# Performance work log

Measured on AMD Instinct MI355X. Metric: run time of the kernel, lower is better.

The kernel has to match this reference:

```python
import jax, jax.numpy as jnp
import numpy as np

BATCH_SIZE = 512
N_PARTS = 4
TEMP_FAC = 0.1
D = 4096
EPS = 1e-6


def _static_indices():
    # bs and factor per the n_parts==4, batch_size!=12 branch
    bs = 4 * BATCH_SIZE
    factor = 10 * N_PARTS
    pos = np.arange(bs)
    active = pos[pos % (3 * N_PARTS) < N_PARTS]            # positions that contribute
    # i1..i6 = (pos + k*n_parts) % bs for k = 0..5
    I = (active[:, None] + np.arange(6)[None, :] * N_PARTS) % bs   # (P, 6)
    # denominator indices removed: (pos + k*n_parts) % bs for k = 0..factor*n_parts-1
    offs = (active[:, None] + np.arange(factor * N_PARTS)[None, :] * N_PARTS) % bs
    M = np.ones((active.shape[0], bs), dtype=np.float32)
    M[np.arange(active.shape[0])[:, None], offs] = 0.0     # (P, bs) denominator mask
    return I, M

_I, _M = _static_indices()
# symmetrical-loss pairs: (i1,i2),(i2,i3),(i1,i4),(i4,i5),(i5,i6),(i2,i5),(i3,i6)
_PAIRS = [(0, 1), (1, 2), (0, 3), (3, 4), (4, 5), (1, 4), (2, 5)]


def setup_inputs() -> dict:
    key = jax.random.key(0)
    reg_pred = jax.random.normal(key, (4 * BATCH_SIZE, D), dtype=jnp.float32)
    return {"reg_pred": reg_pred}


def reference(reg_pred):
    I = jnp.asarray(_I)
    M = jnp.asarray(_M)
    norms = jnp.linalg.norm(reg_pred, axis=1)              # (bs,)
    # torch CosineSimilarity: dot / max(||a||*||b||, eps)
    gram = reg_pred @ reg_pred.T                           # (bs, bs)
    S = gram / jnp.maximum(norms[:, None] * norms[None, :], EPS) / TEMP_FAC
    E = jnp.exp(S)                                         # (bs, bs)
    # denominator exp-sums for each anchor role k at each active position p
    Dsum = jnp.einsum('pkb,pb->pk', E[I], M)               # (P, 6)
    total = jnp.float32(0.0)
    for a, b in _PAIRS:
        num = S[I[:, a], I[:, b]]                          # (P,)
        en = jnp.exp(num)
        total = total + jnp.sum(-jnp.log(en / (en + Dsum[:, a]))
                                - jnp.log(en / (en + Dsum[:, b])))
    return total / (6 * BATCH_SIZE)
```

## Files before the change

kernel.cpp:

```cpp
#include <hip/hip_runtime.h>
#include <hip/hip_bf16.h>
#include <stdint.h>

#define NROWS 2048
#define DIM   4096
#define NACT  684
#define INV_TEMP 10.0f
#define NPANEL 32
#define NTILE64 528
#define NK 64
#define FP8_SCALE 16.0f
#define OUT_SCALE (INV_TEMP / 256.0f)

#define WAITCNT_VM0   0x0F70
#define WAITCNT_VM4   0x0F74
#define WAITCNT_VM8   0x0F78

typedef __attribute__((ext_vector_type(4))) float floatx4;
typedef __attribute__((ext_vector_type(16))) float floatx16;
typedef __attribute__((ext_vector_type(4))) int intx4;
typedef __attribute__((ext_vector_type(8))) int intx8;
typedef __attribute__((ext_vector_type(8))) short shortx8;
typedef __attribute__((ext_vector_type(8))) unsigned short ushortx8;

static __device__ __forceinline__ unsigned short f32_to_bf16(float f) {
  union { float f; unsigned int u; } v; v.f = f;
  unsigned int u = v.u;
  unsigned int r = u + 0x7fffu + ((u >> 16) & 1u);
  return (unsigned short)(r >> 16);
}
static __device__ __forceinline__ float bf16_to_f32(unsigned short u) {
  union { unsigned int u; float f; } v; v.u = ((unsigned int)u) << 16;
  return v.f;
}
static __device__ __forceinline__ unsigned short f32_to_f16(float f) {
  _Float16 h = (_Float16)f;
  union { _Float16 h; unsigned short u; } v; v.h = h;
  return v.u;
}
static __device__ __forceinline__ float f16_to_f32(unsigned short u) {
  union { unsigned short u; _Float16 h; } v; v.u = u;
  return (float)v.h;
}

static __device__ __forceinline__ void num_store(float* __restrict__ NUM, int R, int delta,
                                                 float v) {
  if (delta == 4) {
    const int qs[4]  = {0, 1, 3, 4};
    const int pas[4] = {0, 1, 3, 4};
#pragma unroll
    for (int u = 0; u < 4; u++) {
      const int aa = (R - 4 * pas[u]) & (NROWS - 1);
      if (aa % 12 < 4) NUM[((aa / 12) * 4 + (aa % 12)) * 7 + qs[u]] = v;
    }
  } else {
    const int qs[3]  = {2, 5, 6};
    const int pas[3] = {0, 1, 2};
#pragma unroll
    for (int u = 0; u < 3; u++) {
      const int aa = (R - 4 * pas[u]) & (NROWS - 1);
      if (aa % 12 < 4) NUM[((aa / 12) * 4 + (aa % 12)) * 7 + qs[u]] = v;
    }
  }
}

__global__ __launch_bounds__(256) void k_normconv_fp8(const float* __restrict__ X,
                                                      unsigned char* __restrict__ Yq,
                                                      float* __restrict__ T,
                                                      float* __restrict__ WS,
                                                      float* __restrict__ out) {
  const int row = blockIdx.x;
  if (threadIdx.x == 0) T[row] = 0.f;
  if (row == 0 && threadIdx.x == 64) *out = 0.f;
  if (row < NACT && threadIdx.x >= 192 && threadIdx.x < 198)
    WS[row * 6 + (threadIdx.x - 192)] = 0.f;
  const float4* xr = (const float4*)(X + (size_t)row * DIM);
  float4 v[4];
  float s = 0.f;
#pragma unroll
  for (int t = 0; t < 4; t++) {
    float4 w = xr[threadIdx.x + t * 256];
    v[t] = w;
    s += w.x * w.x + w.y * w.y + w.z * w.z + w.w * w.w;
  }
#pragma unroll
  for (int off = 32; off > 0; off >>= 1) s += __shfl_down(s, off, 64);
  __shared__ float wsum[4];
  if ((threadIdx.x & 63) == 0) wsum[threadIdx.x >> 6] = s;
  __syncthreads();
  const float total = wsum[0] + wsum[1] + wsum[2] + wsum[3];
  const float sc = FP8_SCALE / fmaxf(sqrtf(total), 1e-30f);
  unsigned int* yr = (unsigned int*)(Yq + (size_t)row * DIM);
#pragma unroll
  for (int t = 0; t < 4; t++) {
    float4 w = v[t];
    unsigned int r0 = __builtin_amdgcn_cvt_pk_fp8_f32(w.x * sc, w.y * sc, 0, false);
    r0 = __builtin_amdgcn_cvt_pk_fp8_f32(w.z * sc, w.w * sc, r0, true);
    yr[threadIdx.x + t * 256] = r0;
  }
}

__global__ __launch_bounds__(256) void k_gemm_full(const unsigned char* __restrict__ Yq,
                                                   float* __restrict__ T,
                                                   float* __restrict__ WS,
                                                   float* __restrict__ NUM) {
  __shared__ __attribute__((aligned(16))) unsigned char lds[6 * 8192];
  const int bid0 = blockIdx.x;
  const int t = (bid0 & 7) * 66 + (bid0 >> 3);
  int ti = 0, rem = t;
  while (rem >= NPANEL - ti) { rem -= NPANEL - ti; ti++; }
  const int tj = ti + rem;
  const int gr = ti * 64;
  const int gc = tj * 64;

  const int tid  = threadIdx.x;
  const int lane = tid & 63;
  const int wave = tid >> 6;
  const int wr = wave >> 1;
  const int wc = wave & 1;

  floatx16 acc = {0.f, 0.f, 0.f, 0.f, 0.f, 0.f, 0.f, 0.f,
                  0.f, 0.f, 0.f, 0.f, 0.f, 0.f, 0.f, 0.f};

  const int r2  = tid >> 2;
  const int c16 = tid & 3;
  const unsigned int swst = (unsigned)(((r2 >> 1) & 3) << 4);
  const unsigned int colst = ((unsigned)(c16 << 4)) ^ swst;
  const unsigned char* gA = Yq + (size_t)(gr + r2) * DIM + colst;
  const unsigned char* gB = Yq + (size_t)(gc + r2) * DIM + colst;

#define ISSUE(st, koff)                                                                  \
  do {                                                                                   \
    __builtin_amdgcn_global_load_lds(                                                    \
        (const __attribute__((address_space(1))) void*)(gA + (koff)),                    \
        (__attribute__((address_space(3))) void*)(lds + (st) * 8192 + tid * 16),         \
        16, 0, 0);                                                                       \
    __builtin_amdgcn_global_load_lds(                                                    \
        (const __attribute__((address_space(1))) void*)(gB + (koff)),                    \
        (__attribute__((address_space(3))) void*)(lds + (st) * 8192 + 4096 + tid * 16),  \
        16, 0, 0);                                                                       \
  } while (0)

#define COMPUTE(st)                                                                      \
  do {                                                                                   \
    const unsigned char* bA = lds + (st) * 8192;                                         \
    const unsigned char* bB = bA + 4096;                                                 \
    const unsigned int c0 = (unsigned)((lane >> 5) << 5);                                \
    const int rA = wr * 32 + (lane & 31);                                                \
    const int rB = wc * 32 + (lane & 31);                                                \
    const unsigned int swA = (unsigned)(((rA >> 1) & 3) << 4);                           \
    const unsigned int swB = (unsigned)(((rB >> 1) & 3) << 4);                           \
    const unsigned char* baseA = bA + rA * 64;                                           \
    const unsigned char* baseB = bB + rB * 64;                                           \
    intx4 alo = *(const intx4*)(baseA + (c0 ^ swA));                                     \
    intx4 ahi = *(const intx4*)(baseA + ((c0 ^ swA) ^ 16u));                             \
    intx4 blo = *(const intx4*)(baseB + (c0 ^ swB));                                     \
    intx4 bhi = *(const intx4*)(baseB + ((c0 ^ swB) ^ 16u));                             \
    intx8 af, bf;                                                                        \
    af[0] = alo[0]; af[1] = alo[1]; af[2] = alo[2]; af[3] = alo[3];                      \
    af[4] = ahi[0]; af[5] = ahi[1]; af[6] = ahi[2]; af[7] = ahi[3];                      \
    bf[0] = blo[0]; bf[1] = blo[1]; bf[2] = blo[2]; bf[3] = blo[3];                      \
    bf[4] = bhi[0]; bf[5] = bhi[1]; bf[6] = bhi[2]; bf[7] = bhi[3];                      \
    acc = __builtin_amdgcn_mfma_scale_f32_32x32x64_f8f6f4(                               \
        af, bf, acc, 0, 0, 0, 0x7F7F7F7F, 0, 0x7F7F7F7F);                                \
  } while (0)

  ISSUE(0, 0);
  ISSUE(1, 64);
  ISSUE(2, 128);
  ISSUE(3, 192);
#pragma unroll
  for (int p = 0; p < 32; p++) {
    const int a = (2 * p) % 6;
    if (p < 30) {
      const int na = (2 * p + 4) % 6;
      ISSUE(na, (2 * p + 4) * 64);
      ISSUE(na + 1, (2 * p + 5) * 64);
      __builtin_amdgcn_s_waitcnt(WAITCNT_VM8);
    } else if (p == 30) {
      __builtin_amdgcn_s_waitcnt(WAITCNT_VM4);
    } else {
      __builtin_amdgcn_s_waitcnt(WAITCNT_VM0);
    }
    __builtin_amdgcn_sched_barrier(0);
    __builtin_amdgcn_s_barrier();
    __builtin_amdgcn_s_setprio(1);
    COMPUTE(a);
    COMPUTE(a + 1);
    __builtin_amdgcn_s_setprio(0);
    if (p < 31) {
      __builtin_amdgcn_s_barrier();
      __builtin_amdgcn_sched_barrier(0);
    }
  }

#undef ISSUE
#undef COMPUTE

  float* tileE   = (float*)lds;
  float* colpart = (float*)(lds + 16640);
  __syncthreads();

  {
    const int col = wc * 32 + (lane & 31);
    float evsum = 0.f;
#pragma unroll
    for (int i = 0; i < 16; i++) {
      const int row = wr * 32 + (i & 3) + 8 * (i >> 2) + 4 * (lane >> 5);
      const float v = acc[i] * OUT_SCALE;
      const float ev = __expf(v);
      tileE[row * 65 + col] = ev;
      evsum += ev;
      const int D = (gc + col - gr - row) & (NROWS - 1);
      if (D == 4 || D == 12) num_store(NUM, gr + row, D, v);
      if (ti != tj && (D == 2044 || D == 2036)) num_store(NUM, gc + col, 2048 - D, v);
    }
    evsum += __shfl_xor(evsum, 32, 64);
    if (lane < 32) colpart[wr * 64 + col] = evsum;
  }
  __syncthreads();

  if (tid < 64) {
    const int R = gr + tid;
#pragma unroll
    for (int k = 0; k < 6; k++) {
      const int aa = (R - 4 * k) & (NROWS - 1);
      if (aa % 12 < 4) {
        const int p2 = (aa / 12) * 4 + (aa % 12);
        const int c = aa & 3;
        const int j0 = ((gc >> 2) - (aa >> 2)) & 511;
        float w = 0.f;
#pragma unroll
        for (int i2 = 0; i2 < 16; i2++) {
          const int j = j0 + i2;
          if (j < 160 || j >= 512) w += tileE[tid * 65 + 4 * i2 + c];
        }
        atomicAdd(&WS[p2 * 6 + k], w);
      }
    }
  } else if (tid < 128) {
    if (ti != tj) {
      const int col = tid - 64;
      const int R = gc + col;
#pragma unroll
      for (int k = 0; k < 6; k++) {
        const int aa = (R - 4 * k) & (NROWS - 1);
        if (aa % 12 < 4) {
          const int p2 = (aa / 12) * 4 + (aa % 12);
          const int c = aa & 3;
          const int j0 = ((gr >> 2) - (aa >> 2)) & 511;
          float w = 0.f;
#pragma unroll
          for (int i2 = 0; i2 < 16; i2++) {
            const int j = j0 + i2;
            if (j < 160 || j >= 512) w += tileE[(4 * i2 + c) * 65 + col];
          }
          atomicAdd(&WS[p2 * 6 + k], w);
        }
      }
    }
  } else if (tid < 192) {
    if (ti != tj) {
      const int r = tid - 128;
      float rs = 0.f;
#pragma unroll 8
      for (int c = 0; c < 64; c++) rs += tileE[r * 65 + c];
      atomicAdd(&T[gr + r], rs);
    }
  } else {
    const int c = tid - 192;
    atomicAdd(&T[gc + c], colpart[c] + colpart[64 + c]);
  }
}

__global__ __launch_bounds__(256) void k_finalA(const float* __restrict__ NUM,
                                                const float* __restrict__ WS,
                                                const float* __restrict__ T,
                                                float* __restrict__ out) {
  const int pa[7] = {0, 1, 0, 3, 4, 1, 2};
  const int pb[7] = {1, 2, 3, 4, 5, 4, 5};
  const int idx = blockIdx.x * 256 + threadIdx.x;
  float s = 0.f;
  if (idx < NACT * 7) {
    const int p = idx / 7;
    const int q = idx - p * 7;
    const int a0 = 12 * (p >> 2) + (p & 3);
    const int ra = (a0 + 4 * pa[q]) & (NROWS - 1);
    const int rb = (a0 + 4 * pb[q]) & (NROWS - 1);
    const float dsA = T[ra] - WS[p * 6 + pa[q]];
    const float dsB = T[rb] - WS[p * 6 + pb[q]];
    const float num = NUM[idx];
    const float en = __expf(num);
    s = __logf(en + dsA) + __logf(en + dsB) - 2.f * num;
  }
#pragma unroll
  for (int off = 32; off > 0; off >>= 1) s += __shfl_down(s, off, 64);
  if ((threadIdx.x & 63) == 0) atomicAdd(out, s * (1.0f / (6.0f * 512.0f)));
}

__global__ __launch_bounds__(256) void k_normconv(const float* __restrict__ X,
                                                  unsigned short* __restrict__ Y) {
  const int row = blockIdx.x;
  const float4* xr = (const float4*)(X + (size_t)row * DIM);
  float4 v[4];
  float s = 0.f;
#pragma unroll
  for (int t = 0; t < 4; t++) {
    float4 w = xr[threadIdx.x + t * 256];
    v[t] = w;
    s += w.x * w.x + w.y * w.y + w.z * w.z + w.w * w.w;
  }
#pragma unroll
  for (int off = 32; off > 0; off >>= 1) s += __shfl_down(s, off, 64);
  __shared__ float wsum[4];
  if ((threadIdx.x & 63) == 0) wsum[threadIdx.x >> 6] = s;
  __syncthreads();
  const float total = wsum[0] + wsum[1] + wsum[2] + wsum[3];
  const float inv = 1.0f / fmaxf(sqrtf(total), 1e-30f);
  ushort4* yr = (ushort4*)(Y + (size_t)row * DIM);
#pragma unroll
  for (int t = 0; t < 4; t++) {
    float4 w = v[t];
    ushort4 o;
    o.x = f32_to_bf16(w.x * inv);
    o.y = f32_to_bf16(w.y * inv);
    o.z = f32_to_bf16(w.z * inv);
    o.w = f32_to_bf16(w.w * inv);
    yr[threadIdx.x + t * 256] = o;
  }
}

__global__ __launch_bounds__(256) void k_gemm(const unsigned short* __restrict__ Y,
                                              float* __restrict__ S) {
  __shared__ __attribute__((aligned(16))) unsigned short sA[128 * 32];
  __shared__ __attribute__((aligned(16))) unsigned short sB[128 * 32];
  const int tid  = threadIdx.x;
  const int lane = tid & 63;
  const int wave = tid >> 6;
  const int wr = wave >> 1;
  const int wc = wave & 1;
  const int row0 = blockIdx.y * 128;
  const int col0 = blockIdx.x * 128;

  floatx4 zero = {0.f, 0.f, 0.f, 0.f};
  floatx4 acc[4][4];
#pragma unroll
  for (int i = 0; i < 4; i++)
#pragma unroll
    for (int j = 0; j < 4; j++) acc[i][j] = zero;

  const int sr = tid >> 2;
  const int sc = (tid & 3) * 8;
  const unsigned short* gA0 = Y + (size_t)(row0 + sr) * DIM + sc;
  const unsigned short* gA1 = gA0 + (size_t)64 * DIM;
  const unsigned short* gB0 = Y + (size_t)(col0 + sr) * DIM + sc;
  const unsigned short* gB1 = gB0 + (size_t)64 * DIM;

  const int fr = lane & 15;
  const int fc = (lane >> 4) * 8;

  for (int k0 = 0; k0 < DIM; k0 += 32) {
    __builtin_amdgcn_global_load_lds(
        (const __attribute__((address_space(1))) void*)(gA0 + k0),
        (__attribute__((address_space(3))) void*)(sA + tid * 8), 16, 0, 0);
    __builtin_amdgcn_global_load_lds(
        (const __attribute__((address_space(1))) void*)(gA1 + k0),
        (__attribute__((address_space(3))) void*)(sA + 2048 + tid * 8), 16, 0, 0);
    __builtin_amdgcn_global_load_lds(
        (const __attribute__((address_space(1))) void*)(gB0 + k0),
        (__attribute__((address_space(3))) void*)(sB + tid * 8), 16, 0, 0);
    __builtin_amdgcn_global_load_lds(
        (const __attribute__((address_space(1))) void*)(gB1 + k0),
        (__attribute__((address_space(3))) void*)(sB + 2048 + tid * 8), 16, 0, 0);
    __syncthreads();

    shortx8 af[4], bf[4];
#pragma unroll
    for (int mi = 0; mi < 4; mi++)
      af[mi] = *(const shortx8*)(sA + (wr * 64 + mi * 16 + fr) * 32 + fc);
#pragma unroll
    for (int ni = 0; ni < 4; ni++)
      bf[ni] = *(const shortx8*)(sB + (wc * 64 + ni * 16 + fr) * 32 + fc);
#pragma unroll
    for (int mi = 0; mi < 4; mi++)
#pragma unroll
      for (int ni = 0; ni < 4; ni++)
        acc[mi][ni] = __builtin_amdgcn_mfma_f32_16x16x32_bf16(af[mi], bf[ni], acc[mi][ni], 0, 0, 0);
    __syncthreads();
  }

  const int cc  = lane & 15;
  const int cr4 = (lane >> 4) * 4;
#pragma unroll
  for (int mi = 0; mi < 4; mi++) {
    const int row = row0 + wr * 64 + mi * 16 + cr4;
#pragma unroll
    for (int ni = 0; ni < 4; ni++) {
      const int col = col0 + wc * 64 + ni * 16 + cc;
      float* dst = S + (size_t)row * NROWS + col;
#pragma unroll
      for (int r = 0; r < 4; r++) dst[(size_t)r * NROWS] = acc[mi][ni][r] * INV_TEMP;
    }
  }
}

__global__ __launch_bounds__(256) void k_rowsum(const float* __restrict__ S,
                                                float* __restrict__ T) {
  const int row = blockIdx.x;
  const float* sr = S + (size_t)row * NROWS;
  float s = 0.f;
  for (int b = threadIdx.x; b < NROWS; b += 256) s += __expf(sr[b]);
#pragma unroll
  for (int off = 32; off > 0; off >>= 1) s += __shfl_down(s, off, 64);
  __shared__ float wsum[4];
  if ((threadIdx.x & 63) == 0) wsum[threadIdx.x >> 6] = s;
  __syncthreads();
  if (threadIdx.x == 0) T[row] = wsum[0] + wsum[1] + wsum[2] + wsum[3];
}

__global__ __launch_bounds__(64) void k_dsum(const float* __restrict__ S,
                                             const float* __restrict__ T,
                                             float* __restrict__ Ds) {
  const int p = blockIdx.x;
  const int k = blockIdx.y;
  const int a = 12 * (p >> 2) + (p & 3);
  const int lane = threadIdx.x;
  const int row = (a + 4 * k) & (NROWS - 1);
  const int m = a >> 2;
  const int c = a & 3;
  const float4* sr4 = (const float4*)(S + (size_t)row * NROWS);
  float s = 0.f;
  {
    float4 v0 = sr4[(m + lane) & 511];
    float4 v1 = sr4[(m + 64 + lane) & 511];
    float e0 = c == 0 ? v0.x : c == 1 ? v0.y : c == 2 ? v0.z : v0.w;
    float e1 = c == 0 ? v1.x : c == 1 ? v1.y : c == 2 ? v1.z : v1.w;
    s += __expf(e0) + __expf(e1);
    if (lane < 32) {
      float4 v2 = sr4[(m + 128 + lane) & 511];
      float e2 = c == 0 ? v2.x : c == 1 ? v2.y : c == 2 ? v2.z : v2.w;
      s += __expf(e2);
    }
  }
#pragma unroll
  for (int off = 32; off > 0; off >>= 1) s += __shfl_down(s, off, 64);
  if (lane == 0) Ds[p * 6 + k] = T[row] - s;
}

__global__ __launch_bounds__(256) void k_final(const float* __restrict__ S,
                                               const float* __restrict__ Ds,
                                               float* __restrict__ out) {
  const int pa[7] = {0, 1, 0, 3, 4, 1, 2};
  const int pb[7] = {1, 2, 3, 4, 5, 4, 5};
  const int idx = blockIdx.x * 256 + threadIdx.x;
  float s = 0.f;
  if (idx < NACT * 7) {
    const int p = idx / 7;
    const int q = idx - p * 7;
    const int a0 = 12 * (p >> 2) + (p & 3);
    const int ra = (a0 + 4 * pa[q]) & (NROWS - 1);
    const int rb = (a0 + 4 * pb[q]) & (NROWS - 1);
    const float num = S[(size_t)ra * NROWS + rb];
    const float en = __expf(num);
    s = __logf(en + Ds[p * 6 + pa[q]]) + __logf(en + Ds[p * 6 + pb[q]]) - 2.f * num;
  }
#pragma unroll
  for (int off = 32; off > 0; off >>= 1) s += __shfl_down(s, off, 64);
  if ((threadIdx.x & 63) == 0) atomicAdd(out, s * (1.0f / (6.0f * 512.0f)));
}

extern "C" void kernel_launch(void* const* d_in, const int* in_sizes, int n_in,
                              void* d_out, int out_size, void* d_ws, size_t ws_size,
                              hipStream_t stream) {
  const float* X = (const float*)d_in[0];
  char* ws = (char*)d_ws;
  float* out = (float*)d_out;

  const size_t pOff = (size_t)32 * 1024 * 1024;
  const size_t needA = pOff + 8192 + 24576 + 24576;

  if (ws_size >= needA) {
    unsigned char* Yq = (unsigned char*)ws;
    float* T   = (float*)(ws + pOff);
    float* WS  = (float*)(ws + pOff + 8192);
    float* NUM = (float*)(ws + pOff + 8192 + 24576);
    hipLaunchKernelGGL(k_normconv_fp8, dim3(NROWS), dim3(256), 0, stream, X, Yq, T, WS, out);
    hipLaunchKernelGGL(k_gemm_full, dim3(NTILE64), dim3(256), 0, stream, Yq, T, WS, NUM);
    hipLaunchKernelGGL(k_finalA, dim3((NACT * 7 + 255) / 256), dim3(256), 0, stream,
                       NUM, WS, T, out);
  } else {
    unsigned short* Y = (unsigned short*)ws;
    float* S = (float*)(ws + (size_t)16 * 1024 * 1024);
    float* T  = (float*)(ws + pOff);
    float* Ds = (float*)(ws + pOff + 8192);
    hipMemsetAsync(out, 0, sizeof(float), stream);
    hipLaunchKernelGGL(k_normconv, dim3(NROWS), dim3(256), 0, stream, X, Y);
    hipLaunchKernelGGL(k_gemm, dim3(16, 16), dim3(256), 0, stream, Y, S);
    hipLaunchKernelGGL(k_rowsum, dim3(NROWS), dim3(256), 0, stream, S, T);
    hipLaunchKernelGGL(k_dsum, dim3(NACT, 6), dim3(64), 0, stream, S, T, Ds);
    hipLaunchKernelGGL(k_final, dim3((NACT * 7 + 255) / 256), dim3(256), 0, stream, S, Ds, out);
  }
}
```

Baseline: 105.2 us.

## Switch Gram GEMM to 128x128 tiles with 512 threads and XCD-aware tile map

Replaces the 64x64 upper-triangular tiling (528 blocks, 256 threads) with 128x128 tiles (136 blocks, 512 threads, two 32x32 MFMA accumulators per wave). The tile order comes from a constant lookup table that groups neighbouring tiles onto the same XCD to improve L2 reuse. Larger tiles halve global reads per output element, but 136 blocks leave many of the 256 CUs idle and the LDS footprint doubles. The epilogue reductions are rescaled to the larger tile.

```diff
diff --git a/kernel.cpp b/kernel.cpp
--- a/kernel.cpp
+++ b/kernel.cpp
@@ -6,9 +6,7 @@
 #define DIM   4096
 #define NACT  684
 #define INV_TEMP 10.0f
-#define NPANEL 32
-#define NTILE64 528
-#define NK 64
+#define NTILE128 136
 #define FP8_SCALE 16.0f
 #define OUT_SCALE (INV_TEMP / 256.0f)
 
@@ -22,6 +20,19 @@
 typedef __attribute__((ext_vector_type(8))) int intx8;
 typedef __attribute__((ext_vector_type(8))) short shortx8;
 typedef __attribute__((ext_vector_type(8))) unsigned short ushortx8;
+
+__device__ __constant__ unsigned char TMAP[NTILE128] = {
+  0x00,0x01,0x02,0x03,0x11,0x12,0x13,0x22,0x23,0x33,
+  0x04,0x05,0x06,0x07,0x14,0x15,0x16,0x17,0x24,0x25,0x26,0x27,0x34,0x35,0x36,0x37,
+  0x44,0x45,0x46,0x47,0x55,0x56,0x57,0x66,0x67,0x77,
+  0x48,0x49,0x4A,0x4B,0x58,0x59,0x5A,0x5B,0x68,0x69,0x6A,0x6B,0x78,0x79,0x7A,0x7B,
+  0x88,0x89,0x8A,0x8B,0x99,0x9A,0x9B,0xAA,0xAB,0xBB,
+  0x8C,0x8D,0x8E,0x8F,0x9C,0x9D,0x9E,0x9F,0xAC,0xAD,0xAE,0xAF,0xBC,0xBD,0xBE,0xBF,
+  0xCC,0xCD,0xCE,0xCF,0xDD,0xDE,0xDF,0xEE,0xEF,0xFF,
+  0x0C,0x0D,0x0E,0x0F,0x1C,0x1D,0x1E,0x1F,0x2C,0x2D,0x2E,0x2F,0x3C,0x3D,0x3E,0x3F,
+  0x08,0x09,0x0A,0x0B,0x18,0x19,0x1A,0x1B,0x28,0x29,0x2A,0x2B,0x38,0x39,0x3A,0x3B,
+  0x4C,0x4D,0x4E,0x4F,0x5C,0x5D,0x5E,0x5F,0x6C,0x6D,0x6E,0x6F,0x7C,0x7D,0x7E,0x7F
+};
 
 static __device__ __forceinline__ unsigned short f32_to_bf16(float f) {
   union { float f; unsigned int u; } v; v.f = f;
@@ -100,27 +111,27 @@
   }
 }
 
-__global__ __launch_bounds__(256) void k_gemm_full(const unsigned char* __restrict__ Yq,
+__global__ __launch_bounds__(512) void k_gemm_full(const unsigned char* __restrict__ Yq,
                                                    float* __restrict__ T,
                                                    float* __restrict__ WS,
                                                    float* __restrict__ NUM) {
-  __shared__ __attribute__((aligned(16))) unsigned char lds[6 * 8192];
+  __shared__ __attribute__((aligned(16))) unsigned char lds[6 * 16384];
   const int bid0 = blockIdx.x;
-  const int t = (bid0 & 7) * 66 + (bid0 >> 3);
-  int ti = 0, rem = t;
-  while (rem >= NPANEL - ti) { rem -= NPANEL - ti; ti++; }
-  const int tj = ti + rem;
-  const int gr = ti * 64;
-  const int gc = tj * 64;
+  const int code = TMAP[(bid0 & 7) * 17 + (bid0 >> 3)];
+  const int ti = code >> 4;
+  const int tj = code & 15;
+  const int gr = ti * 128;
+  const int gc = tj * 128;
 
   const int tid  = threadIdx.x;
   const int lane = tid & 63;
   const int wave = tid >> 6;
-  const int wr = wave >> 1;
-  const int wc = wave & 1;
-
-  floatx16 acc = {0.f, 0.f, 0.f, 0.f, 0.f, 0.f, 0.f, 0.f,
-                  0.f, 0.f, 0.f, 0.f, 0.f, 0.f, 0.f, 0.f};
+  const int wr = wave >> 2;
+  const int wc = wave & 3;
+
+  floatx16 zero = {0.f, 0.f, 0.f, 0.f, 0.f, 0.f, 0.f, 0.f,
+                   0.f, 0.f, 0.f, 0.f, 0.f, 0.f, 0.f, 0.f};
+  floatx16 acc0 = zero, acc1 = zero;
 
   const int r2  = tid >> 2;
   const int c16 = tid & 3;
@@ -133,36 +144,45 @@
   do {                                                                                   \
     __builtin_amdgcn_global_load_lds(                                                    \
         (const __attribute__((address_space(1))) void*)(gA + (koff)),                    \
-        (__attribute__((address_space(3))) void*)(lds + (st) * 8192 + tid * 16),         \
+        (__attribute__((address_space(3))) void*)(lds + (st) * 16384 + tid * 16),        \
         16, 0, 0);                                                                       \
     __builtin_amdgcn_global_load_lds(                                                    \
         (const __attribute__((address_space(1))) void*)(gB + (koff)),                    \
-        (__attribute__((address_space(3))) void*)(lds + (st) * 8192 + 4096 + tid * 16),  \
+        (__attribute__((address_space(3))) void*)(lds + (st) * 16384 + 8192 + tid * 16), \
         16, 0, 0);                                                                       \
   } while (0)
 
 #define COMPUTE(st)                                                                      \
   do {                                                                                   \
-    const unsigned char* bA = lds + (st) * 8192;                                         \
-    const unsigned char* bB = bA + 4096;                                                 \
+    const unsigned char* bA = lds + (st) * 16384;                                        \
+    const unsigned char* bB = bA + 8192;                                                 \
     const unsigned int c0 = (unsigned)((lane >> 5) << 5);                                \
-    const int rA = wr * 32 + (lane & 31);                                                \
-    const int rB = wc * 32 + (lane & 31);                                                \
-    const unsigned int swA = (unsigned)(((rA >> 1) & 3) << 4);                           \
-    const unsigned int swB = (unsigned)(((rB >> 1) & 3) << 4);                           \
-    const unsigned char* baseA = bA + rA * 64;                                           \
-    const unsigned char* baseB = bB + rB * 64;                                           \
-    intx4 alo = *(const intx4*)(baseA + (c0 ^ swA));                                     \
-    intx4 ahi = *(const intx4*)(baseA + ((c0 ^ swA) ^ 16u));                             \
-    intx4 blo = *(const intx4*)(baseB + (c0 ^ swB));                                     \
-    intx4 bhi = *(const intx4*)(baseB + ((c0 ^ swB) ^ 16u));                             \
-    intx8 af, bf;                                                                        \
-    af[0] = alo[0]; af[1] = alo[1]; af[2] = alo[2]; af[3] = alo[3];                      \
-    af[4] = ahi[0]; af[5] = ahi[1]; af[6] = ahi[2]; af[7] = ahi[3];                      \
-    bf[0] = blo[0]; bf[1] = blo[1]; bf[2] = blo[2]; bf[3] = blo[3];                      \
-    bf[4] = bhi[0]; bf[5] = bhi[1]; bf[6] = bhi[2]; bf[7] = bhi[3];                      \
-    acc = __builtin_amdgcn_mfma_scale_f32_32x32x64_f8f6f4(                               \
-        af, bf, acc, 0, 0, 0, 0x7F7F7F7F, 0, 0x7F7F7F7F);                                \
+    const int rA0 = wr * 64 + (lane & 31);                                               \
+    const int rA1 = rA0 + 32;                                                            \
+    const int rB  = wc * 32 + (lane & 31);                                               \
+    const unsigned int swA0 = (unsigned)(((rA0 >> 1) & 3) << 4);                         \
+    const unsigned int swA1 = (unsigned)(((rA1 >> 1) & 3) << 4);                         \
+    const unsigned int swB  = (unsigned)(((rB >> 1) & 3) << 4);                          \
+    const unsigned char* baseA0 = bA + rA0 * 64;                                         \
+    const unsigned char* baseA1 = bA + rA1 * 64;                                         \
+    const unsigned char* baseB  = bB + rB * 64;                                          \
+    intx4 a0lo = *(const intx4*)(baseA0 + (c0 ^ swA0));                                  \
+    intx4 a0hi = *(const intx4*)(baseA0 + ((c0 ^ swA0) ^ 16u));                          \
+    intx4 a1lo = *(const intx4*)(baseA1 + (c0 ^ swA1));                                  \
+    intx4 a1hi = *(const intx4*)(baseA1 + ((c0 ^ swA1) ^ 16u));                          \
+    intx4 blo  = *(const intx4*)(baseB + (c0 ^ swB));                                    \
+    intx4 bhi  = *(const intx4*)(baseB + ((c0 ^ swB) ^ 16u));                            \
+    intx8 af0, af1, bf;                                                                  \
+    af0[0] = a0lo[0]; af0[1] = a0lo[1]; af0[2] = a0lo[2]; af0[3] = a0lo[3];              \
+    af0[4] = a0hi[0]; af0[5] = a0hi[1]; af0[6] = a0hi[2]; af0[7] = a0hi[3];              \
+    af1[0] = a1lo[0]; af1[1] = a1lo[1]; af1[2] = a1lo[2]; af1[3] = a1lo[3];              \
+    af1[4] = a1hi[0]; af1[5] = a1hi[1]; af1[6] = a1hi[2]; af1[7] = a1hi[3];              \
+    bf[0]  = blo[0];  bf[1]  = blo[1];  bf[2]  = blo[2];  bf[3]  = blo[3];               \
+    bf[4]  = bhi[0];  bf[5]  = bhi[1];  bf[6]  = bhi[2];  bf[7]  = bhi[3];               \
+    acc0 = __builtin_amdgcn_mfma_scale_f32_32x32x64_f8f6f4(                              \
+        af0, bf, acc0, 0, 0, 0, 0x7F7F7F7F, 0, 0x7F7F7F7F);                              \
+    acc1 = __builtin_amdgcn_mfma_scale_f32_32x32x64_f8f6f4(                              \
+        af1, bf, acc1, 0, 0, 0, 0x7F7F7F7F, 0, 0x7F7F7F7F);                              \
   } while (0)
 
   ISSUE(0, 0);
@@ -198,29 +218,33 @@
 #undef COMPUTE
 
   float* tileE   = (float*)lds;
-  float* colpart = (float*)(lds + 16640);
+  float* colpart = (float*)(lds + 66048);
   __syncthreads();
 
   {
     const int col = wc * 32 + (lane & 31);
     float evsum = 0.f;
 #pragma unroll
-    for (int i = 0; i < 16; i++) {
-      const int row = wr * 32 + (i & 3) + 8 * (i >> 2) + 4 * (lane >> 5);
-      const float v = acc[i] * OUT_SCALE;
-      const float ev = __expf(v);
-      tileE[row * 65 + col] = ev;
-      evsum += ev;
-      const int D = (gc + col - gr - row) & (NROWS - 1);
-      if (D == 4 || D == 12) num_store(NUM, gr + row, D, v);
-      if (ti != tj && (D == 2044 || D == 2036)) num_store(NUM, gc + col, 2048 - D, v);
+    for (int h = 0; h < 2; h++) {
+      const floatx16 a = h ? acc1 : acc0;
+#pragma unroll
+      for (int i = 0; i < 16; i++) {
+        const int row = wr * 64 + h * 32 + (i & 3) + 8 * (i >> 2) + 4 * (lane >> 5);
+        const float v = a[i] * OUT_SCALE;
+        const float ev = __expf(v);
+        tileE[row * 129 + col] = ev;
+        evsum += ev;
+        const int D = (gc + col - gr - row) & (NROWS - 1);
+        if (D == 4 || D == 12) num_store(NUM, gr + row, D, v);
+        if (ti != tj && (D == 2044 || D == 2036)) num_store(NUM, gc + col, 2048 - D, v);
+      }
     }
     evsum += __shfl_xor(evsum, 32, 64);
-    if (lane < 32) colpart[wr * 64 + col] = evsum;
+    if (lane < 32) colpart[wr * 128 + col] = evsum;
   }
   __syncthreads();
 
-  if (tid < 64) {
+  if (tid < 128) {
     const int R = gr + tid;
 #pragma unroll
     for (int k = 0; k < 6; k++) {
@@ -231,16 +255,16 @@
         const int j0 = ((gc >> 2) - (aa >> 2)) & 511;
         float w = 0.f;
 #pragma unroll
-        for (int i2 = 0; i2 < 16; i2++) {
+        for (int i2 = 0; i2 < 32; i2++) {
           const int j = j0 + i2;
-          if (j < 160 || j >= 512) w += tileE[tid * 65 + 4 * i2 + c];
+          if (j < 160 || j >= 512) w += tileE[tid * 129 + 4 * i2 + c];
         }
         atomicAdd(&WS[p2 * 6 + k], w);
       }
     }
-  } else if (tid < 128) {
+  } else if (tid < 256) {
     if (ti != tj) {
-      const int col = tid - 64;
+      const int col = tid - 128;
       const int R = gc + col;
 #pragma unroll
       for (int k = 0; k < 6; k++) {
@@ -251,25 +275,25 @@
           const int j0 = ((gr >> 2) - (aa >> 2)) & 511;
           float w = 0.f;
 #pragma unroll
-          for (int i2 = 0; i2 < 16; i2++) {
+          for (int i2 = 0; i2 < 32; i2++) {
             const int j = j0 + i2;
-            if (j < 160 || j >= 512) w += tileE[(4 * i2 + c) * 65 + col];
+            if (j < 160 || j >= 512) w += tileE[(4 * i2 + c) * 129 + col];
           }
           atomicAdd(&WS[p2 * 6 + k], w);
         }
       }
     }
-  } else if (tid < 192) {
+  } else if (tid < 384) {
     if (ti != tj) {
-      const int r = tid - 128;
+      const int r = tid - 256;
       float rs = 0.f;
 #pragma unroll 8
-      for (int c = 0; c < 64; c++) rs += tileE[r * 65 + c];
+      for (int c = 0; c < 128; c++) rs += tileE[r * 129 + c];
       atomicAdd(&T[gr + r], rs);
     }
   } else {
-    const int c = tid - 192;
-    atomicAdd(&T[gc + c], colpart[c] + colpart[64 + c]);
+    const int c = tid - 384;
+    atomicAdd(&T[gc + c], colpart[c] + colpart[128 + c]);
   }
 }
 
@@ -485,7 +509,7 @@
     float* WS  = (float*)(ws + pOff + 8192);
     float* NUM = (float*)(ws + pOff + 8192 + 24576);
     hipLaunchKernelGGL(k_normconv_fp8, dim3(NROWS), dim3(256), 0, stream, X, Yq, T, WS, out);
-    hipLaunchKernelGGL(k_gemm_full, dim3(NTILE64), dim3(256), 0, stream, Yq, T, WS, NUM);
+    hipLaunchKernelGGL(k_gemm_full, dim3(NTILE128), dim3(512), 0, stream, Yq, T, WS, NUM);
     hipLaunchKernelGGL(k_finalA, dim3((NACT * 7 + 255) / 256), dim3(256), 0, stream,
                        NUM, WS, T, out);
   } else {
```

Measured after the change: 142.1 us. 1.35x slower.

## Use 128x128 split-K FP8 GEMM tiles with separate bf16 partial combine kernel

Applied to the files above, without the earlier changes.

Replaces the 64x64 upper-triangle fused GEMM (528 blocks) with 128x128 tiles split into two K halves (272 blocks), each wave computing a 2x2 grid of 32x32 MFMAs for better LDS operand reuse. Partial results are written to global memory as bf16 and a new 512-thread combine kernel sums them, applies exp and does the row, column and mask reductions. This adds an extra launch, a global round-trip for the partials, and bf16 rounding of the partial dot products before exp.

```diff
diff --git a/kernel.cpp b/kernel.cpp
--- a/kernel.cpp
+++ b/kernel.cpp
@@ -6,11 +6,12 @@
 #define DIM   4096
 #define NACT  684
 #define INV_TEMP 10.0f
-#define NPANEL 32
-#define NTILE64 528
-#define NK 64
+#define NTILE128 136
+#define KSPLIT 2
+#define KSEG  2048
+#define KIT   32
 #define FP8_SCALE 16.0f
-#define OUT_SCALE (INV_TEMP / 256.0f)
+#define PART_SCALE (1.0f / 256.0f)
 
 #define WAITCNT_VM0   0x0F70
 #define WAITCNT_VM4   0x0F74
@@ -100,18 +101,19 @@
   }
 }
 
-__global__ __launch_bounds__(256) void k_gemm_full(const unsigned char* __restrict__ Yq,
-                                                   float* __restrict__ T,
-                                                   float* __restrict__ WS,
-                                                   float* __restrict__ NUM) {
-  __shared__ __attribute__((aligned(16))) unsigned char lds[6 * 8192];
+__global__ __launch_bounds__(256) void k_gemm_mx(const unsigned char* __restrict__ Yq,
+                                                 unsigned short* __restrict__ P) {
+  __shared__ __attribute__((aligned(16))) unsigned char lds[3 * 16384];
   const int bid0 = blockIdx.x;
-  const int t = (bid0 & 7) * 66 + (bid0 >> 3);
+  const int bid = (bid0 & 7) * 34 + (bid0 >> 3);
+  const int kz = bid & 1;
+  const int t  = bid >> 1;
   int ti = 0, rem = t;
-  while (rem >= NPANEL - ti) { rem -= NPANEL - ti; ti++; }
+  while (rem >= 16 - ti) { rem -= 16 - ti; ti++; }
   const int tj = ti + rem;
-  const int gr = ti * 64;
-  const int gc = tj * 64;
+  const int row0 = ti * 128;
+  const int col0 = tj * 128;
+  const int kbase = kz * KSEG;
 
   const int tid  = threadIdx.x;
   const int lane = tid & 63;
@@ -119,76 +121,96 @@
   const int wr = wave >> 1;
   const int wc = wave & 1;
 
-  floatx16 acc = {0.f, 0.f, 0.f, 0.f, 0.f, 0.f, 0.f, 0.f,
-                  0.f, 0.f, 0.f, 0.f, 0.f, 0.f, 0.f, 0.f};
+  floatx16 zero = {0.f, 0.f, 0.f, 0.f, 0.f, 0.f, 0.f, 0.f,
+                   0.f, 0.f, 0.f, 0.f, 0.f, 0.f, 0.f, 0.f};
+  floatx16 acc[2][2];
+#pragma unroll
+  for (int i = 0; i < 2; i++)
+#pragma unroll
+    for (int j = 0; j < 2; j++) acc[i][j] = zero;
 
   const int r2  = tid >> 2;
   const int c16 = tid & 3;
   const unsigned int swst = (unsigned)(((r2 >> 1) & 3) << 4);
   const unsigned int colst = ((unsigned)(c16 << 4)) ^ swst;
-  const unsigned char* gA = Yq + (size_t)(gr + r2) * DIM + colst;
-  const unsigned char* gB = Yq + (size_t)(gc + r2) * DIM + colst;
+  const unsigned char* gA = Yq + (size_t)(row0 + r2) * DIM + kbase + colst;
+  const unsigned char* gB = Yq + (size_t)(col0 + r2) * DIM + kbase + colst;
 
 #define ISSUE(st, koff)                                                                  \
   do {                                                                                   \
     __builtin_amdgcn_global_load_lds(                                                    \
         (const __attribute__((address_space(1))) void*)(gA + (koff)),                    \
-        (__attribute__((address_space(3))) void*)(lds + (st) * 8192 + tid * 16),         \
+        (__attribute__((address_space(3))) void*)(lds + (st) * 16384 + tid * 16),        \
+        16, 0, 0);                                                                       \
+    __builtin_amdgcn_global_load_lds(                                                    \
+        (const __attribute__((address_space(1))) void*)(gA + (size_t)64 * DIM + (koff)), \
+        (__attribute__((address_space(3))) void*)(lds + (st) * 16384 + 4096 + tid * 16), \
         16, 0, 0);                                                                       \
     __builtin_amdgcn_global_load_lds(                                                    \
         (const __attribute__((address_space(1))) void*)(gB + (koff)),                    \
-        (__attribute__((address_space(3))) void*)(lds + (st) * 8192 + 4096 + tid * 16),  \
+        (__attribute__((address_space(3))) void*)(lds + (st) * 16384 + 8192 + tid * 16), \
+        16, 0, 0);                                                                       \
+    __builtin_amdgcn_global_load_lds(                                                    \
+        (const __attribute__((address_space(1))) void*)(gB + (size_t)64 * DIM + (koff)), \
+        (__attribute__((address_space(3))) void*)(lds + (st) * 16384 + 12288 + tid * 16),\
         16, 0, 0);                                                                       \
   } while (0)
 
 #define COMPUTE(st)                                                                      \
   do {                                                                                   \
-    const unsigned char* bA = lds + (st) * 8192;                                         \
-    const unsigned char* bB = bA + 4096;                                                 \
+    const unsigned char* bA = lds + (st) * 16384;                                        \
+    const unsigned char* bB = bA + 8192;                                                 \
     const unsigned int c0 = (unsigned)((lane >> 5) << 5);                                \
-    const int rA = wr * 32 + (lane & 31);                                                \
-    const int rB = wc * 32 + (lane & 31);                                                \
-    const unsigned int swA = (unsigned)(((rA >> 1) & 3) << 4);                           \
-    const unsigned int swB = (unsigned)(((rB >> 1) & 3) << 4);                           \
-    const unsigned char* baseA = bA + rA * 64;                                           \
-    const unsigned char* baseB = bB + rB * 64;                                           \
-    intx4 alo = *(const intx4*)(baseA + (c0 ^ swA));                                     \
-    intx4 ahi = *(const intx4*)(baseA + ((c0 ^ swA) ^ 16u));                             \
-    intx4 blo = *(const intx4*)(baseB + (c0 ^ swB));                                     \
-    intx4 bhi = *(const intx4*)(baseB + ((c0 ^ swB) ^ 16u));                             \
-    intx8 af, bf;                                                                        \
-    af[0] = alo[0]; af[1] = alo[1]; af[2] = alo[2]; af[3] = alo[3];                      \
-    af[4] = ahi[0]; af[5] = ahi[1]; af[6] = ahi[2]; af[7] = ahi[3];                      \
-    bf[0] = blo[0]; bf[1] = blo[1]; bf[2] = blo[2]; bf[3] = blo[3];                      \
-    bf[4] = bhi[0]; bf[5] = bhi[1]; bf[6] = bhi[2]; bf[7] = bhi[3];                      \
-    acc = __builtin_amdgcn_mfma_scale_f32_32x32x64_f8f6f4(                               \
-        af, bf, acc, 0, 0, 0, 0x7F7F7F7F, 0, 0x7F7F7F7F);                                \
+    intx8 af[2], bf[2];                                                                  \
+    _Pragma("unroll")                                                                    \
+    for (int mi = 0; mi < 2; mi++) {                                                     \
+      const int r = wr * 64 + mi * 32 + (lane & 31);                                     \
+      const unsigned int sw = (unsigned)(((r >> 1) & 3) << 4);                           \
+      const unsigned char* base = bA + r * 64;                                           \
+      intx4 lo = *(const intx4*)(base + (c0 ^ sw));                                      \
+      intx4 hi = *(const intx4*)(base + ((c0 ^ sw) ^ 16u));                              \
+      intx8 v;                                                                           \
+      v[0] = lo[0]; v[1] = lo[1]; v[2] = lo[2]; v[3] = lo[3];                            \
+      v[4] = hi[0]; v[5] = hi[1]; v[6] = hi[2]; v[7] = hi[3];                            \
+      af[mi] = v;                                                                        \
+    }                                                                                    \
+    _Pragma("unroll")                                                                    \
+    for (int ni = 0; ni < 2; ni++) {                                                     \
+      const int r = wc * 64 + ni * 32 + (lane & 31);                                     \
+      const unsigned int sw = (unsigned)(((r >> 1) & 3) << 4);                           \
+      const unsigned char* base = bB + r * 64;                                           \
+      intx4 lo = *(const intx4*)(base + (c0 ^ sw));                                      \
+      intx4 hi = *(const intx4*)(base + ((c0 ^ sw) ^ 16u));                              \
+      intx8 v;                                                                           \
+      v[0] = lo[0]; v[1] = lo[1]; v[2] = lo[2]; v[3] = lo[3];                            \
+      v[4] = hi[0]; v[5] = hi[1]; v[6] = hi[2]; v[7] = hi[3];                            \
+      bf[ni] = v;                                                                        \
+    }                                                                                    \
+    _Pragma("unroll")                                                                    \
+    for (int mi = 0; mi < 2; mi++)                                                       \
+      _Pragma("unroll")                                                                  \
+      for (int ni = 0; ni < 2; ni++)                                                     \
+        acc[mi][ni] = __builtin_amdgcn_mfma_scale_f32_32x32x64_f8f6f4(                   \
+            af[mi], bf[ni], acc[mi][ni], 0, 0, 0, 0x7F7F7F7F, 0, 0x7F7F7F7F);            \
   } while (0)
 
   ISSUE(0, 0);
   ISSUE(1, 64);
-  ISSUE(2, 128);
-  ISSUE(3, 192);
-#pragma unroll
-  for (int p = 0; p < 32; p++) {
-    const int a = (2 * p) % 6;
-    if (p < 30) {
-      const int na = (2 * p + 4) % 6;
-      ISSUE(na, (2 * p + 4) * 64);
-      ISSUE(na + 1, (2 * p + 5) * 64);
+#pragma unroll
+  for (int k = 0; k < KIT; k++) {
+    const int cur = k % 3;
+    if (k < KIT - 2) {
+      ISSUE((k + 2) % 3, (k + 2) * 64);
       __builtin_amdgcn_s_waitcnt(WAITCNT_VM8);
-    } else if (p == 30) {
+    } else if (k == KIT - 2) {
       __builtin_amdgcn_s_waitcnt(WAITCNT_VM4);
     } else {
       __builtin_amdgcn_s_waitcnt(WAITCNT_VM0);
     }
     __builtin_amdgcn_sched_barrier(0);
     __builtin_amdgcn_s_barrier();
-    __builtin_amdgcn_s_setprio(1);
-    COMPUTE(a);
-    COMPUTE(a + 1);
-    __builtin_amdgcn_s_setprio(0);
-    if (p < 31) {
+    COMPUTE(cur);
+    if (k < KIT - 1) {
       __builtin_amdgcn_s_barrier();
       __builtin_amdgcn_sched_barrier(0);
     }
@@ -197,79 +219,122 @@
 #undef ISSUE
 #undef COMPUTE
 
-  float* tileE   = (float*)lds;
-  float* colpart = (float*)(lds + 16640);
+  unsigned short* dst = P + (size_t)(t * KSPLIT + kz) * 16384;
+  const int cc = lane & 31;
+  const int cr = (lane >> 5) * 4;
+#pragma unroll
+  for (int mi = 0; mi < 2; mi++) {
+#pragma unroll
+    for (int ni = 0; ni < 2; ni++) {
+      const int col = wc * 64 + ni * 32 + cc;
+#pragma unroll
+      for (int q = 0; q < 4; q++) {
+        const int row = wr * 64 + mi * 32 + q * 8 + cr;
+        unsigned int d0 = (unsigned int)f32_to_bf16(acc[mi][ni][q * 4 + 0] * PART_SCALE) |
+                          ((unsigned int)f32_to_bf16(acc[mi][ni][q * 4 + 1] * PART_SCALE) << 16);
+        unsigned int d1 = (unsigned int)f32_to_bf16(acc[mi][ni][q * 4 + 2] * PART_SCALE) |
+                          ((unsigned int)f32_to_bf16(acc[mi][ni][q * 4 + 3] * PART_SCALE) << 16);
+        uint2 v; v.x = d0; v.y = d1;
+        *(uint2*)(dst + (size_t)col * 128 + row) = v;
+      }
+    }
+  }
+}
+
+__global__ __launch_bounds__(512) void k_combine_full(const unsigned short* __restrict__ P,
+                                                      float* __restrict__ T,
+                                                      float* __restrict__ WS,
+                                                      float* __restrict__ NUM) {
+  __shared__ float tileE[128 * 129];
+  __shared__ float colpart[128];
+  const int t = blockIdx.x;
+  int ti = 0, rem = t;
+  while (rem >= 16 - ti) { rem -= 16 - ti; ti++; }
+  const int tj = ti + rem;
+  const int gr = ti * 128, gc = tj * 128;
+  const int tid = threadIdx.x;
+  const int c = tid >> 2;
+  const int q = tid & 3;
+
+  float evsum = 0.f;
+  {
+    const ushortx8* p0 = (const ushortx8*)(P + (size_t)(t * KSPLIT + 0) * 16384 +
+                                           (size_t)c * 128 + q * 32);
+    const ushortx8* p1 = (const ushortx8*)(P + (size_t)(t * KSPLIT + 1) * 16384 +
+                                           (size_t)c * 128 + q * 32);
+#pragma unroll
+    for (int b = 0; b < 4; b++) {
+      ushortx8 u0 = p0[b];
+      ushortx8 u1 = p1[b];
+#pragma unroll
+      for (int e = 0; e < 8; e++) {
+        const int r = q * 32 + b * 8 + e;
+        const float v = (bf16_to_f32((unsigned short)u0[e]) +
+                         bf16_to_f32((unsigned short)u1[e])) * INV_TEMP;
+        const float ev = __expf(v);
+        tileE[r * 129 + c] = ev;
+        evsum += ev;
+        const int D = (gc + c - gr - r) & (NROWS - 1);
+        if (D == 4 || D == 12) num_store(NUM, gr + r, D, v);
+        if (ti != tj && (D == 2044 || D == 2036)) num_store(NUM, gc + c, 2048 - D, v);
+      }
+    }
+  }
+  evsum += __shfl_xor(evsum, 1, 64);
+  evsum += __shfl_xor(evsum, 2, 64);
+  if (q == 0) colpart[c] = evsum;
   __syncthreads();
 
-  {
-    const int col = wc * 32 + (lane & 31);
-    float evsum = 0.f;
-#pragma unroll
-    for (int i = 0; i < 16; i++) {
-      const int row = wr * 32 + (i & 3) + 8 * (i >> 2) + 4 * (lane >> 5);
-      const float v = acc[i] * OUT_SCALE;
-      const float ev = __expf(v);
-      tileE[row * 65 + col] = ev;
-      evsum += ev;
-      const int D = (gc + col - gr - row) & (NROWS - 1);
-      if (D == 4 || D == 12) num_store(NUM, gr + row, D, v);
-      if (ti != tj && (D == 2044 || D == 2036)) num_store(NUM, gc + col, 2048 - D, v);
-    }
-    evsum += __shfl_xor(evsum, 32, 64);
-    if (lane < 32) colpart[wr * 64 + col] = evsum;
-  }
-  __syncthreads();
-
-  if (tid < 64) {
+  if (tid < 128) {
     const int R = gr + tid;
 #pragma unroll
     for (int k = 0; k < 6; k++) {
       const int aa = (R - 4 * k) & (NROWS - 1);
       if (aa % 12 < 4) {
         const int p2 = (aa / 12) * 4 + (aa % 12);
-        const int c = aa & 3;
+        const int csel = aa & 3;
         const int j0 = ((gc >> 2) - (aa >> 2)) & 511;
         float w = 0.f;
 #pragma unroll
-        for (int i2 = 0; i2 < 16; i2++) {
+        for (int i2 = 0; i2 < 32; i2++) {
           const int j = j0 + i2;
-          if (j < 160 || j >= 512) w += tileE[tid * 65 + 4 * i2 + c];
+          if (j < 160 || j >= 512) w += tileE[tid * 129 + 4 * i2 + csel];
         }
         atomicAdd(&WS[p2 * 6 + k], w);
       }
     }
-  } else if (tid < 128) {
+  } else if (tid < 256) {
     if (ti != tj) {
-      const int col = tid - 64;
+      const int col = tid - 128;
       const int R = gc + col;
 #pragma unroll
       for (int k = 0; k < 6; k++) {
         const int aa = (R - 4 * k) & (NROWS - 1);
         if (aa % 12 < 4) {
           const int p2 = (aa / 12) * 4 + (aa % 12);
-          const int c = aa & 3;
+          const int csel = aa & 3;
           const int j0 = ((gr >> 2) - (aa >> 2)) & 511;
           float w = 0.f;
 #pragma unroll
-          for (int i2 = 0; i2 < 16; i2++) {
+          for (int i2 = 0; i2 < 32; i2++) {
             const int j = j0 + i2;
-            if (j < 160 || j >= 512) w += tileE[(4 * i2 + c) * 65 + col];
+            if (j < 160 || j >= 512) w += tileE[(4 * i2 + csel) * 129 + col];
           }
           atomicAdd(&WS[p2 * 6 + k], w);
         }
       }
     }
-  } else if (tid < 192) {
+  } else if (tid < 384) {
     if (ti != tj) {
-      const int r = tid - 128;
+      const int r = tid - 256;
       float rs = 0.f;
 #pragma unroll 8
-      for (int c = 0; c < 64; c++) rs += tileE[r * 65 + c];
+      for (int cc2 = 0; cc2 < 128; cc2++) rs += tileE[r * 129 + cc2];
       atomicAdd(&T[gr + r], rs);
     }
   } else {
-    const int c = tid - 192;
-    atomicAdd(&T[gc + c], colpart[c] + colpart[64 + c]);
+    const int cc2 = tid - 384;
+    atomicAdd(&T[gc + cc2], colpart[cc2]);
   }
 }
 
@@ -477,15 +542,19 @@
   float* out = (float*)d_out;
 
   const size_t pOff = (size_t)32 * 1024 * 1024;
+  const size_t pBytes = (size_t)NTILE128 * KSPLIT * 16384 * 2;
   const size_t needA = pOff + 8192 + 24576 + 24576;
 
   if (ws_size >= needA) {
     unsigned char* Yq = (unsigned char*)ws;
+    unsigned short* P = (unsigned short*)(ws + (size_t)16 * 1024 * 1024);
     float* T   = (float*)(ws + pOff);
     float* WS  = (float*)(ws + pOff + 8192);
     float* NUM = (float*)(ws + pOff + 8192 + 24576);
+    (void)pBytes;
     hipLaunchKernelGGL(k_normconv_fp8, dim3(NROWS), dim3(256), 0, stream, X, Yq, T, WS, out);
-    hipLaunchKernelGGL(k_gemm_full, dim3(NTILE64), dim3(256), 0, stream, Yq, T, WS, NUM);
+    hipLaunchKernelGGL(k_gemm_mx, dim3(NTILE128 * KSPLIT), dim3(256), 0, stream, Yq, P);
+    hipLaunchKernelGGL(k_combine_full, dim3(NTILE128), dim3(512), 0, stream, P, T, WS, NUM);
     hipLaunchKernelGGL(k_finalA, dim3((NACT * 7 + 255) / 256), dim3(256), 0, stream,
                        NUM, WS, T, out);
   } else {
```

Result: slower. 113.6 us (+8.0%).
